# Performance work log

Hardware: AMD Instinct MI355X
Metric: run time of the kernel (lower is better)

The kernel has to match this reference:

```python
import jax, jax.numpy as jnp
import numpy as np

HEADS = 8
HEAD_DIM = 64
EPS = 1e-5


def setup_inputs() -> dict:
    key = jax.random.key(0)
    k1, k2, k3 = jax.random.split(key, 3)
    dim, hidden = 512, HEADS * HEAD_DIM
    x = jax.random.normal(k1, (8, dim, 64, 64), dtype=jnp.float32)
    w_qkv = jax.random.normal(k2, (hidden * 3, dim), dtype=jnp.float32) * (dim ** -0.5)
    w_out = jax.random.normal(k3, (dim, hidden), dtype=jnp.float32) * (hidden ** -0.5)
    b_out = jnp.zeros((dim,), dtype=jnp.float32)
    g = jnp.ones((dim,), dtype=jnp.float32)
    return {"x": x, "w_qkv": w_qkv, "w_out": w_out, "b_out": b_out, "g": g}


def reference(x, w_qkv, w_out, b_out, g):
    b, c, h, w = x.shape
    n = h * w
    scale = HEAD_DIM ** -0.5
    xf = x.reshape(b, c, n)  # 1x1 conv == channel matmul
    qkv = jnp.einsum('oc,bcn->bon', w_qkv, xf)
    q, k, v = jnp.split(qkv, 3, axis=1)
    def to_heads(t):
        return t.reshape(b, HEADS, HEAD_DIM, n)
    q, k, v = to_heads(q), to_heads(k), to_heads(v)
    q = jax.nn.softmax(q, axis=-2) * scale   # softmax over head_dim
    k = jax.nn.softmax(k, axis=-1)           # softmax over tokens
    v = v / n
    # context: (B,H,d,d) = k (B,H,d,N) @ v^T (B,H,N,e)
    context = jnp.einsum('bhdn,bhen->bhde', k, v)
    # out: context^T (e,d) @ q (d,N) -> (B,H,e,N)
    out = jnp.einsum('bhde,bhdn->bhen', context, q)
    out = out.reshape(b, HEADS * HEAD_DIM, n)
    y = jnp.einsum('co,bon->bcn', w_out, out) + b_out[None, :, None]
    # channel LayerNorm (mean/var over dim=1, biased var, scale g only)
    mean = jnp.mean(y, axis=1, keepdims=True)
    var = jnp.var(y, axis=1, keepdims=True)
    y = (y - mean) * jax.lax.rsqrt(var + EPS) * g[None, :, None]
    return y.reshape(b, c, h, w)
```

## Files before the change

kernel.cpp:

```cpp
#include <hip/hip_runtime.h>
#include <math.h>

#define BB 8
#define NN 4096
#define CD 512
#define HH 8
#define DD 64
#define OC3 1536
#define NSPLIT 16

typedef _Float16 f16;
typedef _Float16 half8 __attribute__((ext_vector_type(8)));
typedef _Float16 half4v __attribute__((ext_vector_type(4)));
typedef float f32x4 __attribute__((ext_vector_type(4)));

__device__ __forceinline__ void gload_lds16(const void* g, void* l) {
    __builtin_amdgcn_global_load_lds(
        (const __attribute__((address_space(1))) unsigned int*)g,
        (__attribute__((address_space(3))) unsigned int*)l, 16, 0, 0);
}

__global__ __launch_bounds__(256) void split_w_kernel(
    const float* __restrict__ w, f16* __restrict__ wh, f16* __restrict__ wl)
{
    int idx = blockIdx.x * 256 + threadIdx.x;
    float4 v = ((const float4*)w)[idx];
    float a[4] = {v.x, v.y, v.z, v.w};
    half4v h, l;
    #pragma unroll
    for (int i = 0; i < 4; ++i) {
        float s = a[i] * 64.f;
        f16 hh = (f16)s;
        h[i] = hh;
        l[i] = (f16)(s - (float)hh);
    }
    *(half4v*)(&wh[(long)idx * 4]) = h;
    *(half4v*)(&wl[(long)idx * 4]) = l;
}

__global__ __launch_bounds__(256) void split_x_kernel(
    const float* __restrict__ x, f16* __restrict__ xth, f16* __restrict__ xtl)
{
    __shared__ float tile[64][65];
    int b = blockIdx.z;
    int n0 = blockIdx.x * 64, c0 = blockIdx.y * 64;
    const float* xb = x + ((long)b * CD + c0) * NN + n0;
    int t = threadIdx.x;
    int tr = t >> 6, tc = t & 63;
    #pragma unroll
    for (int i = 0; i < 16; ++i)
        tile[tr + i * 4][tc] = xb[(long)(tr + i * 4) * NN + tc];
    __syncthreads();

    int nl = t >> 3, ck = (t & 7) * 8;
    long obase = ((long)b * NN + n0) * CD + c0;
    #pragma unroll
    for (int p = 0; p < 2; ++p) {
        int n = nl + p * 32;
        half8 h, l;
        #pragma unroll
        for (int j = 0; j < 8; ++j) {
            float s = tile[ck + j][n] * 16.f;
            f16 hv = (f16)s;
            h[j] = hv;
            l[j] = (f16)(s - (float)hv);
        }
        *(half8*)(&xth[obase + (long)n * CD + ck]) = h;
        *(half8*)(&xtl[obase + (long)n * CD + ck]) = l;
    }
}

#define AR  16384
#define BUF 65536

#define STAGE(Lb, k0s)  do {                                                   \
    long kb_ = (long)(k0s) * 2;                                                \
    _Pragma("unroll")                                                          \
    for (int c_ = 0; c_ < 2; ++c_) {                                           \
        long rowoff_ = (long)(rb0 + c_ * 16) * 1024;                           \
        long ldsoff_ = (long)(rb0 + c_ * 16) * 64;                             \
        gload_lds16(gA_h + rowoff_ + kb_ + g_lane, (Lb) + 0 * AR + ldsoff_);   \
        gload_lds16(gA_l + rowoff_ + kb_ + g_lane, (Lb) + 1 * AR + ldsoff_);   \
        gload_lds16(gB_h + rowoff_ + kb_ + g_lane, (Lb) + 2 * AR + ldsoff_);   \
        gload_lds16(gB_l + rowoff_ + kb_ + g_lane, (Lb) + 3 * AR + ldsoff_);   \
    } } while (0)

__global__ __launch_bounds__(512, 2) void mfma_gemm_kernel(
    const f16* __restrict__ Ah, const f16* __restrict__ Al, long sA,
    const f16* __restrict__ Bh, const f16* __restrict__ Bl, long sB,
    float* __restrict__ Cp, long sC, int ldC, float base_sc)
{
    __shared__ f16 lds[2][4][256 * 32];
    int bz = blockIdx.z;
    int n0 = blockIdx.x * 256, m0 = blockIdx.y * 256;
    int t = threadIdx.x;
    int lane = t & 63, wid = t >> 6;
    int wy = wid >> 2, wx = wid & 3;

    int cl = (lane & 3) ^ ((lane >> 3) & 3);
    long g_lane = (long)(lane >> 2) * 1024 + (long)cl * 16;

    const char* gA_h = (const char*)(Ah + bz * sA) + (long)m0 * 1024;
    const char* gA_l = (const char*)(Al + bz * sA) + (long)m0 * 1024;
    const char* gB_h = (const char*)(Bh + bz * sB) + (long)n0 * 1024;
    const char* gB_l = (const char*)(Bl + bz * sB) + (long)n0 * 1024;

    char* L0 = (char*)&lds[0][0][0];
    int rb0 = wid * 32;

    int cp = (lane >> 4) ^ (((lane & 15) >> 1) & 3);
    long offA = (long)(wy * 128 + (lane & 15)) * 64 + (long)cp * 16;
    long offB = (long)(wx * 64 + (lane & 15)) * 64 + (long)cp * 16;

    f32x4 acc[8][4];
    #pragma unroll
    for (int i = 0; i < 8; ++i)
        #pragma unroll
        for (int j = 0; j < 4; ++j)
            acc[i][j] = (f32x4){0.f, 0.f, 0.f, 0.f};

    STAGE(L0, 0);
    asm volatile("s_waitcnt vmcnt(0)" ::: "memory");
    __syncthreads();

    for (int s = 0; s < 16; ++s) {
        char* Lc = L0 + ((s & 1) ? BUF : 0);
        if (s < 15) {
            char* Ln = L0 + (((s + 1) & 1) ? BUF : 0);
            STAGE(Ln, (s + 1) * 32);
        }

        half8 ah[8], al[8];
        #pragma unroll
        for (int i = 0; i < 8; ++i) {
            ah[i] = *(const half8*)(Lc + 0 * AR + offA + i * 1024);
            al[i] = *(const half8*)(Lc + 1 * AR + offA + i * 1024);
        }
        #pragma unroll
        for (int j = 0; j < 4; ++j) {
            half8 bh = *(const half8*)(Lc + 2 * AR + offB + j * 1024);
            half8 bl = *(const half8*)(Lc + 3 * AR + offB + j * 1024);
            #pragma unroll
            for (int i = 0; i < 8; ++i) {
                acc[i][j] = __builtin_amdgcn_mfma_f32_16x16x32_f16(ah[i], bh, acc[i][j], 0, 0, 0);
                acc[i][j] = __builtin_amdgcn_mfma_f32_16x16x32_f16(ah[i], bl, acc[i][j], 0, 0, 0);
                acc[i][j] = __builtin_amdgcn_mfma_f32_16x16x32_f16(al[i], bh, acc[i][j], 0, 0, 0);
            }
        }

        asm volatile("s_waitcnt vmcnt(0)" ::: "memory");
        __syncthreads();
    }

    int colb = n0 + wx * 64 + (lane & 15);
    int rowb = m0 + wy * 128 + ((lane >> 4) << 2);

    if (m0 < 512) {
        int h0 = (m0 >> 6) + wy * 2;
        f16* qh_b = (f16*)(Cp + (long)bz * sC);
        f16* ql_b = qh_b + (long)CD * NN;
        #pragma unroll
        for (int i = 0; i < 8; ++i)
            #pragma unroll
            for (int j = 0; j < 4; ++j)
                #pragma unroll
                for (int r = 0; r < 4; ++r)
                    acc[i][j][r] *= base_sc;
        #pragma unroll
        for (int j = 0; j < 4; ++j) {
            long nj = colb + j * 16;
            #pragma unroll
            for (int g = 0; g < 2; ++g) {
                float mx = -INFINITY;
                #pragma unroll
                for (int di = 0; di < 4; ++di)
                    #pragma unroll
                    for (int r = 0; r < 4; ++r)
                        mx = fmaxf(mx, acc[g * 4 + di][j][r]);
                mx = fmaxf(mx, __shfl_xor(mx, 16));
                mx = fmaxf(mx, __shfl_xor(mx, 32));
                float sum = 0.f;
                #pragma unroll
                for (int di = 0; di < 4; ++di)
                    #pragma unroll
                    for (int r = 0; r < 4; ++r) {
                        float e = expf(acc[g * 4 + di][j][r] - mx);
                        acc[g * 4 + di][j][r] = e;
                        sum += e;
                    }
                sum += __shfl_xor(sum, 16);
                sum += __shfl_xor(sum, 32);
                float rj = 32.f / sum;
                long off = nj * CD + (h0 + g) * 64 + ((lane >> 4) << 2);
                #pragma unroll
                for (int di = 0; di < 4; ++di) {
                    half4v hh, ll;
                    #pragma unroll
                    for (int r = 0; r < 4; ++r) {
                        float v = acc[g * 4 + di][j][r] * rj;
                        f16 hv = (f16)v;
                        hh[r] = hv;
                        ll[r] = (f16)(v - (float)hv);
                    }
                    *(half4v*)(qh_b + off + di * 16) = hh;
                    *(half4v*)(ql_b + off + di * 16) = ll;
                }
            }
        }
        return;
    }

    if (m0 >= 1024) {
        f16* vhp = (f16*)(Cp + (long)bz * sC + 2L * CD * NN);
        f16* vlp = vhp + (long)CD * NN;
        float vsc = base_sc * 16.f;
        #pragma unroll
        for (int i = 0; i < 8; ++i)
            #pragma unroll
            for (int j = 0; j < 4; ++j)
                #pragma unroll
                for (int r = 0; r < 4; ++r) {
                    long row = rowb + i * 16 + r - 1024;
                    float val = acc[i][j][r] * vsc;
                    f16 hv = (f16)val;
                    vhp[row * NN + colb + j * 16] = hv;
                    vlp[row * NN + colb + j * 16] = (f16)(val - (float)hv);
                }
        return;
    }

    float* outp = Cp + bz * sC;
    #pragma unroll
    for (int i = 0; i < 8; ++i)
        #pragma unroll
        for (int j = 0; j < 4; ++j)
            #pragma unroll
            for (int r = 0; r < 4; ++r) {
                int row = rowb + i * 16 + r;
                outp[(long)row * ldC + colb + j * 16] = acc[i][j][r] * base_sc;
            }
}

#define AR2  8192
#define BUF2 32768

#define STAGE2(Lb, k0s)  do {                                                  \
    long kb_ = (long)(k0s) * 2;                                                \
    _Pragma("unroll")                                                          \
    for (int c_ = 0; c_ < 2; ++c_) {                                           \
        long rowoff_ = (long)(rb0 + c_ * 16) * 1024;                           \
        long ldsoff_ = (long)(rb0 + c_ * 16) * 64;                             \
        gload_lds16(gA_h + rowoff_ + kb_ + g_lane, (Lb) + 0 * AR2 + ldsoff_);  \
        gload_lds16(gA_l + rowoff_ + kb_ + g_lane, (Lb) + 1 * AR2 + ldsoff_);  \
        gload_lds16(gB_h + rowoff_ + kb_ + g_lane, (Lb) + 2 * AR2 + ldsoff_);  \
        gload_lds16(gB_l + rowoff_ + kb_ + g_lane, (Lb) + 3 * AR2 + ldsoff_);  \
    } } while (0)

__global__ __launch_bounds__(256) void mfma_gemm128_kernel(
    const f16* __restrict__ Ah, const f16* __restrict__ Al, long sA,
    const f16* __restrict__ Bh, const f16* __restrict__ Bl, long sB,
    float* __restrict__ Cp, long sC, int ldC,
    const float* __restrict__ bias, const float* __restrict__ inv_sc,
    float base_sc)
{
    __shared__ f16 lds[2][4][128 * 32];
    int bz = blockIdx.z;
    int n0 = blockIdx.x * 128, m0 = blockIdx.y * 128;
    int t = threadIdx.x;
    int lane = t & 63, wid = t >> 6;
    int wy = wid >> 1, wx = wid & 1;

    int cl = (lane & 3) ^ ((lane >> 3) & 3);
    long g_lane = (long)(lane >> 2) * 1024 + (long)cl * 16;

    const char* gA_h = (const char*)(Ah + bz * sA) + (long)m0 * 1024;
    const char* gA_l = (const char*)(Al + bz * sA) + (long)m0 * 1024;
    const char* gB_h = (const char*)(Bh + bz * sB) + (long)n0 * 1024;
    const char* gB_l = (const char*)(Bl + bz * sB) + (long)n0 * 1024;

    char* L0 = (char*)&lds[0][0][0];
    int rb0 = wid * 32;

    int cp = (lane >> 4) ^ (((lane & 15) >> 1) & 3);
    long offA = (long)(wy * 64 + (lane & 15)) * 64 + (long)cp * 16;
    long offB = (long)(wx * 64 + (lane & 15)) * 64 + (long)cp * 16;

    f32x4 acc[4][4];
    #pragma unroll
    for (int i = 0; i < 4; ++i)
        #pragma unroll
        for (int j = 0; j < 4; ++j)
            acc[i][j] = (f32x4){0.f, 0.f, 0.f, 0.f};

    STAGE2(L0, 0);
    asm volatile("s_waitcnt vmcnt(0)" ::: "memory");
    __syncthreads();

    for (int s = 0; s < 16; ++s) {
        char* Lc = L0 + ((s & 1) ? BUF2 : 0);
        if (s < 15) {
            char* Ln = L0 + (((s + 1) & 1) ? BUF2 : 0);
            STAGE2(Ln, (s + 1) * 32);
        }

        half8 ah[4], al[4], bh[4], bl[4];
        #pragma unroll
        for (int i = 0; i < 4; ++i) {
            ah[i] = *(const half8*)(Lc + 0 * AR2 + offA + i * 1024);
            al[i] = *(const half8*)(Lc + 1 * AR2 + offA + i * 1024);
            bh[i] = *(const half8*)(Lc + 2 * AR2 + offB + i * 1024);
            bl[i] = *(const half8*)(Lc + 3 * AR2 + offB + i * 1024);
        }
        #pragma unroll
        for (int i = 0; i < 4; ++i)
            #pragma unroll
            for (int j = 0; j < 4; ++j) {
                acc[i][j] = __builtin_amdgcn_mfma_f32_16x16x32_f16(ah[i], bh[j], acc[i][j], 0, 0, 0);
                acc[i][j] = __builtin_amdgcn_mfma_f32_16x16x32_f16(ah[i], bl[j], acc[i][j], 0, 0, 0);
                acc[i][j] = __builtin_amdgcn_mfma_f32_16x16x32_f16(al[i], bh[j], acc[i][j], 0, 0, 0);
            }

        asm volatile("s_waitcnt vmcnt(0)" ::: "memory");
        __syncthreads();
    }

    int colb = n0 + wx * 64 + (lane & 15);
    int rowb = m0 + wy * 64 + ((lane >> 4) << 2);
    float* outp = Cp + bz * sC;
    float mult = base_sc * (inv_sc ? inv_sc[bz] : 1.f);
    #pragma unroll
    for (int i = 0; i < 4; ++i)
        #pragma unroll
        for (int j = 0; j < 4; ++j)
            #pragma unroll
            for (int r = 0; r < 4; ++r) {
                int row = rowb + i * 16 + r;
                float bb = bias ? bias[row] : 0.f;
                outp[(long)row * ldC + colb + j * 16] = acc[i][j][r] * mult + bb;
            }
}

__global__ __launch_bounds__(256) void k_rowstat_kernel(
    const float* __restrict__ qkv, float* __restrict__ statmx,
    float* __restrict__ statinv)
{
    int row = blockIdx.x;
    int b = row >> 9;
    int hd = row & (CD - 1);
    const float* base = qkv + ((long)b * OC3 + CD + hd) * NN;
    int t = threadIdx.x;

    float v[16];
    #pragma unroll
    for (int i = 0; i < 16; ++i) v[i] = base[t + i * 256];

    __shared__ float red[256];
    float mx = -INFINITY;
    #pragma unroll
    for (int i = 0; i < 16; ++i) mx = fmaxf(mx, v[i]);
    red[t] = mx; __syncthreads();
    for (int off = 128; off > 0; off >>= 1) {
        if (t < off) red[t] = fmaxf(red[t], red[t + off]);
        __syncthreads();
    }
    mx = red[0]; __syncthreads();

    float s = 0.f;
    #pragma unroll
    for (int i = 0; i < 16; ++i) {
        v[i] = expf(v[i] - mx);
        s += v[i];
    }
    red[t] = s; __syncthreads();
    for (int off = 128; off > 0; off >>= 1) {
        if (t < off) red[t] += red[t + off];
        __syncthreads();
    }
    if (t == 0) {
        statmx[row] = mx;
        statinv[row] = 4096.f / red[0];
    }
}

__global__ __launch_bounds__(256) void ctx_mfma_kernel(
    const float* __restrict__ qkv, const float* __restrict__ statmx,
    const float* __restrict__ statinv, float* __restrict__ ctxp)
{
    __shared__ char lds[16384];
    int sp = blockIdx.x;
    int bh = blockIdx.y;
    int b = bh >> 3, h = bh & 7;
    int t = threadIdx.x, lane = t & 63, w = t >> 6;

    const char* kg = (const char*)(qkv + ((long)b * OC3 + CD + (long)h * 64) * NN);
    const char* vhg = (const char*)(qkv + ((long)b * OC3 + 2L * CD) * NN) + (long)h * 64 * (NN * 2);
    const char* vlg = vhg + (long)CD * NN * 2;

    int lr = lane & 15, hi = lane >> 4;
    float mx[4], inv[4];
    #pragma unroll
    for (int i = 0; i < 4; ++i) {
        int ridx = b * CD + h * 64 + i * 16 + lr;
        mx[i] = statmx[ridx];
        inv[i] = statinv[ridx];
    }

    int cl = (lane & 3) ^ ((lane >> 3) & 3);
    int cp16 = (hi ^ ((lr >> 1) & 3)) * 16;

    int ksrow = (lane >> 3);
    int ksc = lane & 7;

    f32x4 acc[4];
    #pragma unroll
    for (int i = 0; i < 4; ++i) acc[i] = (f32x4){0.f, 0.f, 0.f, 0.f};

    int s7 = lr & 7;

    for (int ks = 0; ks < 8; ++ks) {
        int n0 = sp * 256 + ks * 32;
        if (w < 2) {
            #pragma unroll
            for (int it2 = 0; it2 < 4; ++it2) {
                int it = w * 4 + it2;
                int r = it * 8 + ksrow;
                gload_lds16(kg + (long)r * (NN * 4) + (long)n0 * 4 + ((ksc ^ (r & 7)) << 4),
                            lds + it * 1024 + lane * 16);
            }
        } else {
            const char* gv = (w == 2) ? vhg : vlg;
            char* lv = lds + 8192 + (w - 2) * 4096;
            #pragma unroll
            for (int c2 = 0; c2 < 4; ++c2)
                gload_lds16(gv + (long)(c2 * 16 + (lane >> 2)) * (NN * 2) + (long)n0 * 2 + (long)cl * 16,
                            lv + c2 * 1024 + lane * 16);
        }
        asm volatile("s_waitcnt vmcnt(0)" ::: "memory");
        __syncthreads();

        half8 ah[4], al[4];
        #pragma unroll
        for (int i = 0; i < 4; ++i) {
            int row = i * 16 + lr;
            const char* rb = lds + row * 128;
            f32x4 a0 = *(const f32x4*)(rb + (((2 * hi) ^ s7) << 4));
            f32x4 a1 = *(const f32x4*)(rb + (((2 * hi + 1) ^ s7) << 4));
            #pragma unroll
            for (int j = 0; j < 8; ++j) {
                float kv = (j < 4) ? a0[j] : a1[j - 4];
                float e = expf(kv - mx[i]) * inv[i];
                f16 hv = (f16)e;
                ah[i][j] = hv;
                al[i][j] = (f16)(e - (float)hv);
            }
        }
        half8 bhf = *(const half8*)(lds + 8192 + (w * 16 + lr) * 64 + cp16);
        half8 blf = *(const half8*)(lds + 12288 + (w * 16 + lr) * 64 + cp16);
        #pragma unroll
        for (int i = 0; i < 4; ++i) {
            acc[i] = __builtin_amdgcn_mfma_f32_16x16x32_f16(ah[i], bhf, acc[i], 0, 0, 0);
            acc[i] = __builtin_amdgcn_mfma_f32_16x16x32_f16(ah[i], blf, acc[i], 0, 0, 0);
            acc[i] = __builtin_amdgcn_mfma_f32_16x16x32_f16(al[i], bhf, acc[i], 0, 0, 0);
        }
        __syncthreads();
    }

    float* op = ctxp + ((long)bh * NSPLIT + sp) * 4096;
    #pragma unroll
    for (int i = 0; i < 4; ++i)
        #pragma unroll
        for (int r = 0; r < 4; ++r)
            op[(i * 16 + hi * 4 + r) * 64 + w * 16 + lr] = acc[i][r];
}

__global__ __launch_bounds__(256) void fold_wout_kernel(
    const float* __restrict__ w_out, const float* __restrict__ ctxp,
    float* __restrict__ Mf)
{
    __shared__ float cl[64][65];
    int bh = blockIdx.x;
    int b = bh >> 3, h = bh & 7;
    int t = threadIdx.x;
    const float* cp = ctxp + (long)bh * NSPLIT * 4096;
    #pragma unroll
    for (int i = 0; i < 16; ++i) {
        int de = t + i * 256;
        double s = 0.0;
        #pragma unroll
        for (int sp = 0; sp < NSPLIT; ++sp)
            s += (double)cp[(long)sp * 4096 + de];
        cl[de >> 6][de & 63] = (float)(s * (1.0 / 268435456.0));
    }
    __syncthreads();

    int d = t & 63, tc = t >> 6;
    for (int ci = 0; ci < 128; ++ci) {
        int c = tc * 128 + ci;
        const float* wr = w_out + (long)c * CD + h * DD;
        float s = 0.f;
        #pragma unroll
        for (int e = 0; e < 64; ++e) s += wr[e] * cl[d][e];
        Mf[((long)b * CD + c) * CD + h * DD + d] = s;
    }
}

__global__ __launch_bounds__(256) void max_m_part_kernel(
    const float* __restrict__ Mf, float* __restrict__ part)
{
    int blk = blockIdx.x;
    int b = blk >> 5, sub = blk & 31;
    const float4* p = (const float4*)(Mf + (long)b * CD * CD) + (long)sub * 2048;
    float mx = 0.f;
    for (int i = threadIdx.x; i < 2048; i += 256) {
        float4 v = p[i];
        mx = fmaxf(mx, fmaxf(fmaxf(fabsf(v.x), fabsf(v.y)),
                             fmaxf(fabsf(v.z), fabsf(v.w))));
    }
    __shared__ float red[256];
    red[threadIdx.x] = mx; __syncthreads();
    for (int off = 128; off > 0; off >>= 1) {
        if (threadIdx.x < off) red[threadIdx.x] = fmaxf(red[threadIdx.x], red[threadIdx.x + off]);
        __syncthreads();
    }
    if (threadIdx.x == 0) part[blk] = red[0];
}

__global__ __launch_bounds__(64) void max_m_final_kernel(
    const float* __restrict__ part, float* __restrict__ scl)
{
    int b = threadIdx.x;
    if (b < 8) {
        float m = 0.f;
        #pragma unroll
        for (int i = 0; i < 32; ++i) m = fmaxf(m, part[b * 32 + i]);
        int e = (m > 1e-30f) ? ilogbf(m) : 0;
        scl[b] = ldexpf(1.f, 10 - e);
        scl[8 + b] = ldexpf(1.f, e - 10);
    }
}

__global__ __launch_bounds__(256) void split_m_kernel(
    const float* __restrict__ Mf, const float* __restrict__ scl,
    f16* __restrict__ mh, f16* __restrict__ ml)
{
    int idx = blockIdx.x * 256 + threadIdx.x;
    float s = scl[idx >> 16];
    float4 v = ((const float4*)Mf)[idx];
    float a[4] = {v.x, v.y, v.z, v.w};
    half4v h, l;
    #pragma unroll
    for (int i = 0; i < 4; ++i) {
        float tval = a[i] * s;
        f16 hv = (f16)tval;
        h[i] = hv;
        l[i] = (f16)(tval - (float)hv);
    }
    *(half4v*)(&mh[(long)idx * 4]) = h;
    *(half4v*)(&ml[(long)idx * 4]) = l;
}

__global__ __launch_bounds__(256) void layernorm_kernel(
    const float* __restrict__ qkv, const float* __restrict__ g,
    float* __restrict__ out)
{
    int t = threadIdx.x;
    int tn = t & 31, cy = t >> 5;
    long col = (long)blockIdx.x * 32 + tn;
    int n = (int)(col & (NN - 1));
    int b = (int)(col >> 12);
    const float* base = qkv + (long)b * OC3 * NN + (long)CD * NN + n;

    float v[64];
    double s = 0.0, ss = 0.0;
    #pragma unroll
    for (int i = 0; i < 64; ++i) {
        v[i] = base[(long)(cy * 64 + i) * NN];
        s += (double)v[i];
        ss += (double)v[i] * (double)v[i];
    }

    __shared__ double rs[8][32], rss[8][32];
    rs[cy][tn] = s; rss[cy][tn] = ss;
    __syncthreads();
    __shared__ float mb[32], ib[32];
    if (cy == 0) {
        double S = 0.0, SS = 0.0;
        #pragma unroll
        for (int j = 0; j < 8; ++j) { S += rs[j][tn]; SS += rss[j][tn]; }
        double mean = S * (1.0 / CD);
        double var = SS * (1.0 / CD) - mean * mean;
        mb[tn] = (float)mean;
        ib[tn] = (float)(1.0 / sqrt(var + 1e-5));
    }
    __syncthreads();
    float m = mb[tn], iv = ib[tn];

    float* oc = out + (long)b * CD * NN + n;
    #pragma unroll
    for (int i = 0; i < 64; ++i)
        oc[(long)(cy * 64 + i) * NN] = (v[i] - m) * iv * g[cy * 64 + i];
}

extern "C" void kernel_launch(void* const* d_in, const int* in_sizes, int n_in,
                              void* d_out, int out_size, void* d_ws, size_t ws_size,
                              hipStream_t stream)
{
    const float* x     = (const float*)d_in[0];
    const float* w_qkv = (const float*)d_in[1];
    const float* w_out = (const float*)d_in[2];
    const float* b_out = (const float*)d_in[3];
    const float* g     = (const float*)d_in[4];
    float* out = (float*)d_out;

    float* ws   = (float*)d_ws;
    float* qkv  = ws;
    float* ctxp = qkv + (long)BB * OC3 * NN;
    f16*   mh   = (f16*)(ctxp + (long)BB * HH * NSPLIT * DD * DD);
    f16*   ml   = mh + (long)BB * CD * CD;
    f16*   wh   = (f16*)(ml + (long)BB * CD * CD);
    f16*   wl   = wh + (long)OC3 * CD;
    float* scl  = (float*)(wl + (long)OC3 * CD);
    float* part = scl + 16;
    float* statmx = part + 256;
    float* statinv = statmx + BB * CD;

    f16* xth = (f16*)d_out;
    f16* xtl = xth + (long)BB * NN * CD;
    float* Mf = (float*)d_out;

    split_w_kernel<<<(OC3 * CD / 4) / 256, 256, 0, stream>>>(w_qkv, wh, wl);
    split_x_kernel<<<dim3(NN / 64, CD / 64, BB), 256, 0, stream>>>(x, xth, xtl);

    mfma_gemm_kernel<<<dim3(NN / 256, OC3 / 256, BB), 512, 0, stream>>>(
        wh, wl, 0L, xth, xtl, (long)NN * CD,
        qkv, (long)OC3 * NN, NN, 1.0f / 1024.0f);

    k_rowstat_kernel<<<BB * CD, 256, 0, stream>>>(qkv, statmx, statinv);

    ctx_mfma_kernel<<<dim3(NSPLIT, BB * HH), 256, 0, stream>>>(
        qkv, statmx, statinv, ctxp);

    fold_wout_kernel<<<BB * HH, 256, 0, stream>>>(w_out, ctxp, Mf);
    max_m_part_kernel<<<256, 256, 0, stream>>>(Mf, part);
    max_m_final_kernel<<<1, 64, 0, stream>>>(part, scl);
    split_m_kernel<<<(BB * CD * CD / 4) / 256, 256, 0, stream>>>(Mf, scl, mh, ml);

    mfma_gemm128_kernel<<<dim3(NN / 128, CD / 128, BB), 256, 0, stream>>>(
        mh, ml, (long)CD * CD,
        (const f16*)qkv, (const f16*)qkv + (long)CD * NN, (long)OC3 * NN * 2,
        qkv + (long)CD * NN, (long)OC3 * NN, NN, b_out, scl + 8, 1.0f / 256.0f);

    layernorm_kernel<<<(BB * NN) / 32, 256, 0, stream>>>(qkv, g, out);
}
```

Baseline: 434.7 us.

## Fuse output projection GEMM with channel LayerNorm in one kernel

Replaces the second GEMM plus the separate LayerNorm kernel with one kernel whose 512-thread block computes all 512 output channels for a 128-column tile. Per-column mean and variance are then reduced in LDS and the normalized result is written straight to the output. This removes the fp32 round trip of y through global memory and one kernel launch. The A operand (mh/ml) is now read directly from global memory into registers rather than staged in LDS. Occupancy drops to one large block per CU and the grid shrinks to 256 blocks, with 128 accumulator vectors per thread.

```diff
diff --git a/kernel.cpp b/kernel.cpp
--- a/kernel.cpp
+++ b/kernel.cpp
@@ -241,105 +241,6 @@
             }
 }
 
-#define AR2  8192
-#define BUF2 32768
-
-#define STAGE2(Lb, k0s)  do {                                                  \
-    long kb_ = (long)(k0s) * 2;                                                \
-    _Pragma("unroll")                                                          \
-    for (int c_ = 0; c_ < 2; ++c_) {                                           \
-        long rowoff_ = (long)(rb0 + c_ * 16) * 1024;                           \
-        long ldsoff_ = (long)(rb0 + c_ * 16) * 64;                             \
-        gload_lds16(gA_h + rowoff_ + kb_ + g_lane, (Lb) + 0 * AR2 + ldsoff_);  \
-        gload_lds16(gA_l + rowoff_ + kb_ + g_lane, (Lb) + 1 * AR2 + ldsoff_);  \
-        gload_lds16(gB_h + rowoff_ + kb_ + g_lane, (Lb) + 2 * AR2 + ldsoff_);  \
-        gload_lds16(gB_l + rowoff_ + kb_ + g_lane, (Lb) + 3 * AR2 + ldsoff_);  \
-    } } while (0)
-
-__global__ __launch_bounds__(256) void mfma_gemm128_kernel(
-    const f16* __restrict__ Ah, const f16* __restrict__ Al, long sA,
-    const f16* __restrict__ Bh, const f16* __restrict__ Bl, long sB,
-    float* __restrict__ Cp, long sC, int ldC,
-    const float* __restrict__ bias, const float* __restrict__ inv_sc,
-    float base_sc)
-{
-    __shared__ f16 lds[2][4][128 * 32];
-    int bz = blockIdx.z;
-    int n0 = blockIdx.x * 128, m0 = blockIdx.y * 128;
-    int t = threadIdx.x;
-    int lane = t & 63, wid = t >> 6;
-    int wy = wid >> 1, wx = wid & 1;
-
-    int cl = (lane & 3) ^ ((lane >> 3) & 3);
-    long g_lane = (long)(lane >> 2) * 1024 + (long)cl * 16;
-
-    const char* gA_h = (const char*)(Ah + bz * sA) + (long)m0 * 1024;
-    const char* gA_l = (const char*)(Al + bz * sA) + (long)m0 * 1024;
-    const char* gB_h = (const char*)(Bh + bz * sB) + (long)n0 * 1024;
-    const char* gB_l = (const char*)(Bl + bz * sB) + (long)n0 * 1024;
-
-    char* L0 = (char*)&lds[0][0][0];
-    int rb0 = wid * 32;
-
-    int cp = (lane >> 4) ^ (((lane & 15) >> 1) & 3);
-    long offA = (long)(wy * 64 + (lane & 15)) * 64 + (long)cp * 16;
-    long offB = (long)(wx * 64 + (lane & 15)) * 64 + (long)cp * 16;
-
-    f32x4 acc[4][4];
-    #pragma unroll
-    for (int i = 0; i < 4; ++i)
-        #pragma unroll
-        for (int j = 0; j < 4; ++j)
-            acc[i][j] = (f32x4){0.f, 0.f, 0.f, 0.f};
-
-    STAGE2(L0, 0);
-    asm volatile("s_waitcnt vmcnt(0)" ::: "memory");
-    __syncthreads();
-
-    for (int s = 0; s < 16; ++s) {
-        char* Lc = L0 + ((s & 1) ? BUF2 : 0);
-        if (s < 15) {
-            char* Ln = L0 + (((s + 1) & 1) ? BUF2 : 0);
-            STAGE2(Ln, (s + 1) * 32);
-        }
-
-        half8 ah[4], al[4], bh[4], bl[4];
-        #pragma unroll
-        for (int i = 0; i < 4; ++i) {
-            ah[i] = *(const half8*)(Lc + 0 * AR2 + offA + i * 1024);
-            al[i] = *(const half8*)(Lc + 1 * AR2 + offA + i * 1024);
-            bh[i] = *(const half8*)(Lc + 2 * AR2 + offB + i * 1024);
-            bl[i] = *(const half8*)(Lc + 3 * AR2 + offB + i * 1024);
-        }
-        #pragma unroll
-        for (int i = 0; i < 4; ++i)
-            #pragma unroll
-            for (int j = 0; j < 4; ++j) {
-                acc[i][j] = __builtin_amdgcn_mfma_f32_16x16x32_f16(ah[i], bh[j], acc[i][j], 0, 0, 0);
-                acc[i][j] = __builtin_amdgcn_mfma_f32_16x16x32_f16(ah[i], bl[j], acc[i][j], 0, 0, 0);
-                acc[i][j] = __builtin_amdgcn_mfma_f32_16x16x32_f16(al[i], bh[j], acc[i][j], 0, 0, 0);
-            }
-
-        asm volatile("s_waitcnt vmcnt(0)" ::: "memory");
-        __syncthreads();
-    }
-
-    int colb = n0 + wx * 64 + (lane & 15);
-    int rowb = m0 + wy * 64 + ((lane >> 4) << 2);
-    float* outp = Cp + bz * sC;
-    float mult = base_sc * (inv_sc ? inv_sc[bz] : 1.f);
-    #pragma unroll
-    for (int i = 0; i < 4; ++i)
-        #pragma unroll
-        for (int j = 0; j < 4; ++j)
-            #pragma unroll
-            for (int r = 0; r < 4; ++r) {
-                int row = rowb + i * 16 + r;
-                float bb = bias ? bias[row] : 0.f;
-                outp[(long)row * ldC + colb + j * 16] = acc[i][j][r] * mult + bb;
-            }
-}
-
 __global__ __launch_bounds__(256) void k_rowstat_kernel(
     const float* __restrict__ qkv, float* __restrict__ statmx,
     float* __restrict__ statinv)
@@ -559,46 +460,134 @@
     *(half4v*)(&ml[(long)idx * 4]) = l;
 }
 
-__global__ __launch_bounds__(256) void layernorm_kernel(
-    const float* __restrict__ qkv, const float* __restrict__ g,
-    float* __restrict__ out)
-{
-    int t = threadIdx.x;
-    int tn = t & 31, cy = t >> 5;
-    long col = (long)blockIdx.x * 32 + tn;
-    int n = (int)(col & (NN - 1));
-    int b = (int)(col >> 12);
-    const float* base = qkv + (long)b * OC3 * NN + (long)CD * NN + n;
-
-    float v[64];
-    double s = 0.0, ss = 0.0;
-    #pragma unroll
-    for (int i = 0; i < 64; ++i) {
-        v[i] = base[(long)(cy * 64 + i) * NN];
-        s += (double)v[i];
-        ss += (double)v[i] * (double)v[i];
-    }
-
-    __shared__ double rs[8][32], rss[8][32];
-    rs[cy][tn] = s; rss[cy][tn] = ss;
+#define GB_AR 8192
+#define GB_BUF 16384
+
+__global__ __launch_bounds__(512, 1) void gemm2_ln_kernel(
+    const f16* __restrict__ mh, const f16* __restrict__ ml,
+    const f16* __restrict__ qh0, const f16* __restrict__ ql0, long sB,
+    const float* __restrict__ b_out, const float* __restrict__ g,
+    const float* __restrict__ inv_sc, float base_sc, float* __restrict__ out)
+{
+    __shared__ char lds[2 * GB_BUF + 32768 + 1024];
+    double* reds  = (double*)(lds + 2 * GB_BUF);
+    double* redss = (double*)(lds + 2 * GB_BUF + 16384);
+    float* meanb  = (float*)(lds + 2 * GB_BUF + 32768);
+    float* invb   = meanb + 128;
+
+    int bz = blockIdx.z;
+    int n0 = blockIdx.x * 128;
+    int t = threadIdx.x, lane = t & 63, wid = t >> 6;
+    int wy = wid >> 1, wx = wid & 1;
+    int lr = lane & 15, hi = lane >> 4;
+
+    int cl = (lane & 3) ^ ((lane >> 3) & 3);
+    long g_lane = (long)(lane >> 2) * 1024 + (long)cl * 16;
+    const char* gB_h = (const char*)(qh0 + bz * sB) + (long)n0 * 1024;
+    const char* gB_l = (const char*)(ql0 + bz * sB) + (long)n0 * 1024;
+    int brow = wid * 16;
+
+    int cp = hi ^ ((lr >> 1) & 3);
+    long offB = (long)(wx * 64 + lr) * 64 + (long)cp * 16;
+
+    const char* gAh = (const char*)(mh + (long)bz * CD * CD) + (long)(wy * 128 + lr) * 1024 + hi * 16;
+    const char* gAl = (const char*)(ml + (long)bz * CD * CD) + (long)(wy * 128 + lr) * 1024 + hi * 16;
+
+    f32x4 acc[8][4];
+    #pragma unroll
+    for (int i = 0; i < 8; ++i)
+        #pragma unroll
+        for (int j = 0; j < 4; ++j)
+            acc[i][j] = (f32x4){0.f, 0.f, 0.f, 0.f};
+
+    {
+        char* Lb = lds;
+        gload_lds16(gB_h + (long)brow * 1024 + g_lane, Lb + 0 * GB_AR + (long)brow * 64);
+        gload_lds16(gB_l + (long)brow * 1024 + g_lane, Lb + 1 * GB_AR + (long)brow * 64);
+    }
+    asm volatile("s_waitcnt vmcnt(0)" ::: "memory");
     __syncthreads();
-    __shared__ float mb[32], ib[32];
-    if (cy == 0) {
+
+    for (int s = 0; s < 16; ++s) {
+        char* Lc = lds + ((s & 1) ? GB_BUF : 0);
+        if (s < 15) {
+            char* Ln = lds + (((s + 1) & 1) ? GB_BUF : 0);
+            long kb = (long)(s + 1) * 64;
+            gload_lds16(gB_h + (long)brow * 1024 + kb + g_lane, Ln + 0 * GB_AR + (long)brow * 64);
+            gload_lds16(gB_l + (long)brow * 1024 + kb + g_lane, Ln + 1 * GB_AR + (long)brow * 64);
+        }
+
+        long kb = (long)s * 64;
+        half8 ah[8], al[8];
+        #pragma unroll
+        for (int i = 0; i < 8; ++i) {
+            ah[i] = *(const half8*)(gAh + (long)i * 16384 + kb);
+            al[i] = *(const half8*)(gAl + (long)i * 16384 + kb);
+        }
+        #pragma unroll
+        for (int j = 0; j < 4; ++j) {
+            half8 bh = *(const half8*)(Lc + 0 * GB_AR + offB + j * 1024);
+            half8 bl = *(const half8*)(Lc + 1 * GB_AR + offB + j * 1024);
+            #pragma unroll
+            for (int i = 0; i < 8; ++i) {
+                acc[i][j] = __builtin_amdgcn_mfma_f32_16x16x32_f16(ah[i], bh, acc[i][j], 0, 0, 0);
+                acc[i][j] = __builtin_amdgcn_mfma_f32_16x16x32_f16(ah[i], bl, acc[i][j], 0, 0, 0);
+                acc[i][j] = __builtin_amdgcn_mfma_f32_16x16x32_f16(al[i], bh, acc[i][j], 0, 0, 0);
+            }
+        }
+
+        asm volatile("s_waitcnt vmcnt(0)" ::: "memory");
+        __syncthreads();
+    }
+
+    float mult = base_sc * inv_sc[bz];
+    int contrib = wy * 4 + hi;
+    #pragma unroll
+    for (int j = 0; j < 4; ++j) {
+        double sum = 0.0, ss = 0.0;
+        #pragma unroll
+        for (int i = 0; i < 8; ++i)
+            #pragma unroll
+            for (int r = 0; r < 4; ++r) {
+                int row = wy * 128 + i * 16 + hi * 4 + r;
+                float y = acc[i][j][r] * mult + b_out[row];
+                acc[i][j][r] = y;
+                sum += (double)y;
+                ss += (double)y * (double)y;
+            }
+        int col = wx * 64 + j * 16 + lr;
+        reds[col * 16 + contrib] = sum;
+        redss[col * 16 + contrib] = ss;
+    }
+    __syncthreads();
+
+    if (t < 128) {
         double S = 0.0, SS = 0.0;
         #pragma unroll
-        for (int j = 0; j < 8; ++j) { S += rs[j][tn]; SS += rss[j][tn]; }
+        for (int c2 = 0; c2 < 16; ++c2) {
+            S += reds[t * 16 + c2];
+            SS += redss[t * 16 + c2];
+        }
         double mean = S * (1.0 / CD);
         double var = SS * (1.0 / CD) - mean * mean;
-        mb[tn] = (float)mean;
-        ib[tn] = (float)(1.0 / sqrt(var + 1e-5));
+        meanb[t] = (float)mean;
+        invb[t] = (float)(1.0 / sqrt(var + 1e-5));
     }
     __syncthreads();
-    float m = mb[tn], iv = ib[tn];
-
-    float* oc = out + (long)b * CD * NN + n;
-    #pragma unroll
-    for (int i = 0; i < 64; ++i)
-        oc[(long)(cy * 64 + i) * NN] = (v[i] - m) * iv * g[cy * 64 + i];
+
+    #pragma unroll
+    for (int j = 0; j < 4; ++j) {
+        int col = wx * 64 + j * 16 + lr;
+        float m = meanb[col], iv = invb[col];
+        int n = n0 + col;
+        #pragma unroll
+        for (int i = 0; i < 8; ++i)
+            #pragma unroll
+            for (int r = 0; r < 4; ++r) {
+                int row = wy * 128 + i * 16 + hi * 4 + r;
+                out[((long)bz * CD + row) * NN + n] = (acc[i][j][r] - m) * iv * g[row];
+            }
+    }
 }
 
 extern "C" void kernel_launch(void* const* d_in, const int* in_sizes, int n_in,
@@ -645,10 +634,8 @@
     max_m_final_kernel<<<1, 64, 0, stream>>>(part, scl);
     split_m_kernel<<<(BB * CD * CD / 4) / 256, 256, 0, stream>>>(Mf, scl, mh, ml);
 
-    mfma_gemm128_kernel<<<dim3(NN / 128, CD / 128, BB), 256, 0, stream>>>(
-        mh, ml, (long)CD * CD,
+    gemm2_ln_kernel<<<dim3(NN / 128, 1, BB), 512, 0, stream>>>(
+        mh, ml,
         (const f16*)qkv, (const f16*)qkv + (long)CD * NN, (long)OC3 * NN * 2,
-        qkv + (long)CD * NN, (long)OC3 * NN, NN, b_out, scl + 8, 1.0f / 256.0f);
-
-    layernorm_kernel<<<(BB * NN) / 32, 256, 0, stream>>>(qkv, g, out);
-}
+        b_out, g, scl + 8, 1.0f / 256.0f, out);
+}
```

Result: slower. 443.4 us (+2.0%).

## Split context reduction into its own kernel and widen fold_wout grid

Applied to the files above, without the earlier changes.

The split-K context partial sums are now reduced by a separate fully parallel kernel into a compact ctx buffer. fold_wout then only loads the reduced context and runs across 4x more blocks (256 instead of 64), each covering a quarter of the output channels, with a partially unrolled inner loop. This targets the low occupancy and serial work of the old 64-block fold kernel. The cost is an extra launch and a round trip through memory, and Mf is moved to reuse the ctxp workspace.

```diff
diff --git a/kernel.cpp b/kernel.cpp
--- a/kernel.cpp
+++ b/kernel.cpp
@@ -473,29 +473,40 @@
             op[(i * 16 + hi * 4 + r) * 64 + w * 16 + lr] = acc[i][r];
 }
 
+__global__ __launch_bounds__(256) void context_reduce_kernel(
+    const float* __restrict__ ctxp, float* __restrict__ ctx)
+{
+    int idx = blockIdx.x * 256 + threadIdx.x;
+    int bh = idx >> 12;
+    int de = idx & 4095;
+    double s = 0.0;
+    #pragma unroll
+    for (int sp = 0; sp < NSPLIT; ++sp)
+        s += (double)ctxp[((long)bh * NSPLIT + sp) * 4096 + de];
+    ctx[idx] = (float)(s * (1.0 / 268435456.0));
+}
+
 __global__ __launch_bounds__(256) void fold_wout_kernel(
-    const float* __restrict__ w_out, const float* __restrict__ ctxp,
+    const float* __restrict__ w_out, const float* __restrict__ ctx,
     float* __restrict__ Mf)
 {
     __shared__ float cl[64][65];
-    int bh = blockIdx.x;
+    int ct = blockIdx.x;
+    int bh = blockIdx.y;
     int b = bh >> 3, h = bh & 7;
     int t = threadIdx.x;
-    const float* cp = ctxp + (long)bh * NSPLIT * 4096;
+    const float* cp = ctx + (long)bh * 4096;
     #pragma unroll
     for (int i = 0; i < 16; ++i) {
-        int de = t + i * 256;
-        double s = 0.0;
-        #pragma unroll
-        for (int sp = 0; sp < NSPLIT; ++sp)
-            s += (double)cp[(long)sp * 4096 + de];
-        cl[de >> 6][de & 63] = (float)(s * (1.0 / 268435456.0));
+        int o = t + i * 256;
+        cl[o >> 6][o & 63] = cp[o];
     }
     __syncthreads();
 
     int d = t & 63, tc = t >> 6;
-    for (int ci = 0; ci < 128; ++ci) {
-        int c = tc * 128 + ci;
+    #pragma unroll 4
+    for (int ci = 0; ci < 32; ++ci) {
+        int c = ct * 128 + tc * 32 + ci;
         const float* wr = w_out + (long)c * CD + h * DD;
         float s = 0.f;
         #pragma unroll
@@ -615,7 +626,8 @@
     float* ws   = (float*)d_ws;
     float* qkv  = ws;
     float* ctxp = qkv + (long)BB * OC3 * NN;
-    f16*   mh   = (f16*)(ctxp + (long)BB * HH * NSPLIT * DD * DD);
+    float* ctx  = ctxp + (long)BB * HH * NSPLIT * DD * DD;
+    f16*   mh   = (f16*)(ctx + (long)BB * HH * DD * DD);
     f16*   ml   = mh + (long)BB * CD * CD;
     f16*   wh   = (f16*)(ml + (long)BB * CD * CD);
     f16*   wl   = wh + (long)OC3 * CD;
@@ -623,10 +635,10 @@
     float* part = scl + 16;
     float* statmx = part + 256;
     float* statinv = statmx + BB * CD;
+    float* Mf   = ctxp;
 
     f16* xth = (f16*)d_out;
     f16* xtl = xth + (long)BB * NN * CD;
-    float* Mf = (float*)d_out;
 
     split_w_kernel<<<(OC3 * CD / 4) / 256, 256, 0, stream>>>(w_qkv, wh, wl);
     split_x_kernel<<<dim3(NN / 64, CD / 64, BB), 256, 0, stream>>>(x, xth, xtl);
@@ -639,8 +651,9 @@
 
     ctx_mfma_kernel<<<dim3(NSPLIT, BB * HH), 256, 0, stream>>>(
         qkv, statmx, statinv, ctxp);
-
-    fold_wout_kernel<<<BB * HH, 256, 0, stream>>>(w_out, ctxp, Mf);
+    context_reduce_kernel<<<(BB * HH * DD * DD) / 256, 256, 0, stream>>>(ctxp, ctx);
+
+    fold_wout_kernel<<<dim3(4, BB * HH), 256, 0, stream>>>(w_out, ctx, Mf);
     max_m_part_kernel<<<256, 256, 0, stream>>>(Mf, part);
     max_m_final_kernel<<<1, 64, 0, stream>>>(part, scl);
     split_m_kernel<<<(BB * CD * CD / 4) / 256, 256, 0, stream>>>(Mf, scl, mh, ml);
```

After: 376.5 us. -13.4%, faster.
